# Kernel tuning notes

Measured on AMD Instinct MI355X. Metric: run time of the kernel, lower is better.

## Reference

```python
import jax, jax.numpy as jnp
import numpy as np

N_NODES = 50000
N_EDGES = 800000
D_IN = 128
D_HID = 128
BN_EPS = 1e-5


def _sage_mean(h, src, dst, w_self, w_neigh, b):
    # DGL SAGEConv('mean'): out = h @ W_self + mean_{neighbors}(h_src) @ W_neigh + bias
    msg = h[src]                                               # [E, D] gather
    ssum = jax.ops.segment_sum(msg, dst, num_segments=N_NODES)  # [N, D]
    deg = jax.ops.segment_sum(jnp.ones((src.shape[0],), h.dtype), dst,
                              num_segments=N_NODES)            # [N]
    mean = ssum / jnp.maximum(deg, 1.0)[:, None]
    return h @ w_self + mean @ w_neigh + b


def _bn_relu(h, gamma, beta):
    # BatchNorm1d with batch statistics (training-mode math), then ReLU.
    m = jnp.mean(h, axis=0)
    v = jnp.mean(jnp.square(h - m), axis=0)  # biased variance, as torch uses for normalization
    hn = (h - m) * jax.lax.rsqrt(v + BN_EPS) * gamma + beta
    return jax.nn.relu(hn)


def setup_inputs() -> dict:
    key = jax.random.key(0)
    ks = jax.random.split(key, 16)
    x = jax.random.normal(ks[0], (N_NODES, D_IN), dtype=jnp.float32)
    src = jax.random.randint(ks[1], (N_EDGES,), 0, N_NODES, dtype=jnp.int32)
    dst = jax.random.randint(ks[2], (N_EDGES,), 0, N_NODES, dtype=jnp.int32)
    s0 = 1.0 / np.sqrt(D_IN)
    s1 = 1.0 / np.sqrt(D_HID)
    inp = {
        'x': x, 'src': src, 'dst': dst,
        'W_self0': jax.random.uniform(ks[3], (D_IN, D_HID), jnp.float32, -s0, s0),
        'W_neigh0': jax.random.uniform(ks[4], (D_IN, D_HID), jnp.float32, -s0, s0),
        'b0': jnp.zeros((D_HID,), jnp.float32),
        'W_self1': jax.random.uniform(ks[5], (D_HID, D_HID), jnp.float32, -s1, s1),
        'W_neigh1': jax.random.uniform(ks[6], (D_HID, D_HID), jnp.float32, -s1, s1),
        'b1': jnp.zeros((D_HID,), jnp.float32),
        'W_self2': jax.random.uniform(ks[7], (D_HID, D_HID), jnp.float32, -s1, s1),
        'W_neigh2': jax.random.uniform(ks[8], (D_HID, D_HID), jnp.float32, -s1, s1),
        'b2': jnp.zeros((D_HID,), jnp.float32),
        'gamma0': jnp.ones((D_HID,), jnp.float32),
        'beta0': jnp.zeros((D_HID,), jnp.float32),
        'gamma1': jnp.ones((D_HID,), jnp.float32),
        'beta1': jnp.zeros((D_HID,), jnp.float32),
    }
    return inp


def reference(x, src, dst,
              W_self0, W_neigh0, b0,
              W_self1, W_neigh1, b1,
              W_self2, W_neigh2, b2,
              gamma0, beta0, gamma1, beta1):
    h = _sage_mean(x, src, dst, W_self0, W_neigh0, b0)
    h = _bn_relu(h, gamma0, beta0)  # dropout is identity in eval mode
    h = _sage_mean(h, src, dst, W_self1, W_neigh1, b1)
    h = _bn_relu(h, gamma1, beta1)
    h = _sage_mean(h, src, dst, W_self2, W_neigh2, b2)
    return h
```

## Files before the change

kernel.cpp:

```cpp
#include <hip/hip_runtime.h>

#define N_NODES 50000
#define N_EDGES 800000
#define D 128
#define BN_EPS 1e-5f

#define NBUCK 391
#define BSHIFT 7
#define S1_BLOCKS 256
#define EPB 3125
#define CVT_BLOCKS 6250
#define PACK_BLOCKS 384
#define NREP 16
#define NSLICE 8
#define SSHIFT 13
#define BN_BLOCKS 512

typedef __attribute__((ext_vector_type(8))) short bf16x8;
typedef __attribute__((ext_vector_type(4))) float f32x4;
typedef __attribute__((ext_vector_type(2))) float f32x2;

__device__ inline unsigned short f2bf(float f) {
    unsigned int u = __float_as_uint(f);
    u = (u + 0x7FFF + ((u >> 16) & 1)) >> 16;
    return (unsigned short)u;
}

__device__ inline float bf2f(unsigned short b) {
    return __uint_as_float(((unsigned)b) << 16);
}

__device__ __forceinline__ void acc_plain(f32x2* a, uint4 v) {
    unsigned w[4] = {v.x, v.y, v.z, v.w};
#pragma unroll
    for (int p = 0; p < 4; p++) {
        f32x2 f;
        f.x = __uint_as_float(w[p] << 16);
        f.y = __uint_as_float(w[p] & 0xffff0000u);
        a[p] += f;
    }
}


__global__ void fused_prep(const float* __restrict__ x, unsigned short* __restrict__ x16,
                           const int* __restrict__ dst, int* __restrict__ hist,
                           const float* __restrict__ Ws0, const float* __restrict__ Wn0,
                           const float* __restrict__ Ws1, const float* __restrict__ Wn1,
                           const float* __restrict__ Ws2, const float* __restrict__ Wn2,
                           unsigned short* __restrict__ Wf, float* __restrict__ statsg) {
    __shared__ int lh[NBUCK];
    const int bid = blockIdx.x, t = threadIdx.x;

    if (bid < CVT_BLOCKS) {
        int idx = bid * 256 + t;
        float4 v = ((const float4*)x)[idx];
        ushort4 o;
        o.x = f2bf(v.x); o.y = f2bf(v.y); o.z = f2bf(v.z); o.w = f2bf(v.w);
        ((ushort4*)x16)[idx] = o;
    } else if (bid < CVT_BLOCKS + S1_BLOCKS) {
        int blk = bid - CVT_BLOCKS;
        for (int i = t; i < NBUCK; i += 256) lh[i] = 0;
        __syncthreads();
        int e0 = blk * EPB;
        for (int i = 0; i < 13; i++) {
            int k = t + i * 256;
            if (k < EPB) atomicAdd(&lh[dst[e0 + k] >> BSHIFT], 1);
        }
        __syncthreads();
        for (int i = t; i < NBUCK; i += 256) hist[blk * NBUCK + i] = lh[i];
    } else {
        if (bid == CVT_BLOCKS + S1_BLOCKS) {
            for (int i = t; i < 2 * NREP * 256; i += 256) statsg[i] = 0.f;
        }
        int idx = (bid - (CVT_BLOCKS + S1_BLOCKS)) * 256 + t;
        if (idx < 3 * 32768) {
            int layer = idx >> 15;
            int rem = idx & 32767;
            int kt = rem >> 12;
            int nt = (rem >> 9) & 7;
            int lane = (rem >> 3) & 63;
            int j = rem & 7;
            int k = kt * 32 + (lane >> 4) * 8 + j;
            int n = nt * 16 + (lane & 15);
            const float* Wsrc;
            if (layer == 0) Wsrc = (k < 128) ? Ws0 : Wn0;
            else if (layer == 1) Wsrc = (k < 128) ? Ws1 : Wn1;
            else Wsrc = (k < 128) ? Ws2 : Wn2;
            Wf[idx] = f2bf(Wsrc[(k & 127) * D + n]);
        }
    }
}


__global__ void s2a(int* __restrict__ hist, int* __restrict__ bucketTotal) {
    __shared__ int s[S1_BLOCKS];
    int b = blockIdx.x, t = threadIdx.x;
    int v = hist[t * NBUCK + b];
    s[t] = v;
    __syncthreads();
    for (int off = 1; off < S1_BLOCKS; off <<= 1) {
        int x = (t >= off) ? s[t - off] : 0;
        __syncthreads();
        s[t] += x;
        __syncthreads();
    }
    hist[t * NBUCK + b] = s[t] - v;
    if (t == S1_BLOCKS - 1) bucketTotal[b] = s[t];
}


__global__ void s3_scatter(const int* __restrict__ src, const int* __restrict__ dst,
                           const int* __restrict__ hist, const int* __restrict__ bucketTotal,
                           int* __restrict__ bucketStart, unsigned int* __restrict__ rec) {
    __shared__ int sc[512];
    __shared__ int base[NBUCK];
    int blk = blockIdx.x, t = threadIdx.x;
    int i1 = t + 256;
    int v0 = (t < NBUCK) ? bucketTotal[t] : 0;
    int v1 = (i1 < NBUCK) ? bucketTotal[i1] : 0;
    sc[t] = v0; sc[i1] = v1;
    __syncthreads();
    for (int off = 1; off < 512; off <<= 1) {
        int x0 = (t >= off) ? sc[t - off] : 0;
        int x1 = (i1 >= off) ? sc[i1 - off] : 0;
        __syncthreads();
        sc[t] += x0; sc[i1] += x1;
        __syncthreads();
    }
    if (t < NBUCK)  base[t]  = (sc[t] - v0)  + hist[blk * NBUCK + t];
    if (i1 < NBUCK) base[i1] = (sc[i1] - v1) + hist[blk * NBUCK + i1];
    if (blk == 0) {
        if (t < NBUCK)  bucketStart[t]  = sc[t] - v0;
        if (i1 < NBUCK) bucketStart[i1] = sc[i1] - v1;
        if (t == 0) bucketStart[NBUCK] = N_EDGES;
    }
    __syncthreads();
    int e0 = blk * EPB;
    for (int i = 0; i < 13; i++) {
        int k = t + i * 256;
        if (k < EPB) {
            int e = e0 + k;
            int d = dst[e];
            int p = atomicAdd(&base[d >> BSHIFT], 1);
            rec[p] = ((unsigned)(d & 127) << 16) | (unsigned)src[e];
        }
    }
}


__global__ void s4_build(const unsigned int* __restrict__ rec, const int* __restrict__ bucketStart,
                         unsigned short* __restrict__ csr, int* __restrict__ degi,
                         int* __restrict__ offsets, float* __restrict__ inv_deg) {
    __shared__ int cnt[128 * NSLICE];
    __shared__ int exc[128 * NSLICE];
    __shared__ int lcur[128 * NSLICE];
    __shared__ int ls[256];
    int b = blockIdx.x, t = threadIdx.x;
    int start = bucketStart[b], end = bucketStart[b + 1];

    for (int i = t; i < 128 * NSLICE; i += 256) cnt[i] = 0;
    __syncthreads();
    for (int e = start + t; e < end; e += 256) {
        unsigned r = rec[e];
        int key = ((r >> 16) << 3) | ((r & 0xFFFFu) >> SSHIFT);
        atomicAdd(&cnt[key], 1);
    }
    __syncthreads();

    int c0 = cnt[4 * t], c1 = cnt[4 * t + 1], c2 = cnt[4 * t + 2], c3 = cnt[4 * t + 3];
    int sum4 = c0 + c1 + c2 + c3;
    ls[t] = sum4;
    __syncthreads();
    for (int off = 1; off < 256; off <<= 1) {
        int x = (t >= off) ? ls[t - off] : 0;
        __syncthreads();
        ls[t] += x;
        __syncthreads();
    }
    int base = ls[t] - sum4;
    exc[4 * t]     = base;
    exc[4 * t + 1] = base + c0;
    exc[4 * t + 2] = base + c0 + c1;
    exc[4 * t + 3] = base + c0 + c1 + c2;
    lcur[4 * t]     = start + base;
    lcur[4 * t + 1] = start + base + c0;
    lcur[4 * t + 2] = start + base + c0 + c1;
    lcur[4 * t + 3] = start + base + c0 + c1 + c2;
    __syncthreads();

    if (t < 128) {
        int node = (b << BSHIFT) + t;
        int e0 = exc[8 * t];
        int e1 = (t == 127) ? (end - start) : exc[8 * t + 8];
        int v = e1 - e0;
        if (node < N_NODES) {
            degi[node] = v;
            offsets[node] = start + e0;
            inv_deg[node] = 1.0f / (float)max(v, 1);
        }
    }
    __syncthreads();
    for (int e = start + t; e < end; e += 256) {
        unsigned r = rec[e];
        int key = ((r >> 16) << 3) | ((r & 0xFFFFu) >> SSHIFT);
        int p = atomicAdd(&lcur[key], 1);
        csr[p] = (unsigned short)(r & 0xFFFFu);
    }
}


__global__ void degsort(const int* __restrict__ degi, int* __restrict__ perm) {
    __shared__ int h[256];
    __shared__ int cur[256];
    int t = threadIdx.x;
    if (t < 256) h[t] = 0;
    __syncthreads();
    for (int i = t; i < N_NODES; i += 1024)
        atomicAdd(&h[255 - min(degi[i], 255)], 1);
    __syncthreads();
    int v = (t < 256) ? h[t] : 0;
    for (int off = 1; off < 256; off <<= 1) {
        int x = 0;
        if (t < 256 && t >= off) x = h[t - off];
        __syncthreads();
        if (t < 256) h[t] += x;
        __syncthreads();
    }
    if (t < 256) cur[t] = h[t] - v;
    __syncthreads();
    for (int i = t; i < N_NODES; i += 1024) {
        int b = 255 - min(degi[i], 255);
        perm[atomicAdd(&cur[b], 1)] = i;
    }
}


__global__ void bn_relu_apply(unsigned short* __restrict__ h,
                              const float* __restrict__ stats,
                              const float* __restrict__ gamma, const float* __restrict__ beta) {
    __shared__ float sc[128], sh[128];
    int t = threadIdx.x;
    if (t < 128) {
        const float invN = 1.0f / (float)N_NODES;
        float s = 0.f, q = 0.f;
#pragma unroll
        for (int r = 0; r < NREP; r++) {
            s += stats[r * 256 + t];
            q += stats[r * 256 + 128 + t];
        }
        float m = s * invN;
        float var = q * invN - m * m;
        float scv = rsqrtf(var + BN_EPS) * gamma[t];
        sc[t] = scv;
        sh[t] = beta[t] - m * scv;
    }
    __syncthreads();
    const int total = N_NODES * D / 8;
    for (int idx = blockIdx.x * 256 + t; idx < total; idx += BN_BLOCKS * 256) {
        uint4 v = ((const uint4*)h)[idx];
        int col0 = (idx & 15) * 8;
        unsigned w[4] = {v.x, v.y, v.z, v.w};
        unsigned ow[4];
#pragma unroll
        for (int p = 0; p < 4; p++) {
            float lo = __uint_as_float(w[p] << 16);
            float hi = __uint_as_float(w[p] & 0xffff0000u);
            float rlo = fmaxf(lo * sc[col0 + 2 * p]     + sh[col0 + 2 * p],     0.f);
            float rhi = fmaxf(hi * sc[col0 + 2 * p + 1] + sh[col0 + 2 * p + 1], 0.f);
            ow[p] = ((unsigned)f2bf(rhi) << 16) | f2bf(rlo);
        }
        uint4 o;
        o.x = ow[0]; o.y = ow[1]; o.z = ow[2]; o.w = ow[3];
        ((uint4*)h)[idx] = o;
    }
}


#define GATHER(k) (*(const uint4*)(hb + ((size_t)csr[beg + (k)] << 7)))

__global__ void aggregate16(const unsigned short* __restrict__ h16,
                            const unsigned short* __restrict__ csr, const int* __restrict__ offsets,
                            const int* __restrict__ degi, const float* __restrict__ inv_deg,
                            const int* __restrict__ perm,
                            unsigned short* __restrict__ mean16) {
    int t = threadIdx.x;
    int node = perm[blockIdx.x * 16 + (t >> 4)];
    int c = t & 15;
    const unsigned short* hb = h16 + c * 8;
    int beg = offsets[node], n = degi[node];
    f32x2 a[4];
#pragma unroll
    for (int j = 0; j < 4; j++) a[j] = (f32x2)(0.f);

    int i = 0;
    if (n >= 4) {
        uint4 v0 = GATHER(0), v1 = GATHER(1), v2 = GATHER(2), v3 = GATHER(3);
        for (i = 4; i + 3 < n; i += 4) {
            uint4 w0 = GATHER(i), w1 = GATHER(i + 1), w2 = GATHER(i + 2), w3 = GATHER(i + 3);
            acc_plain(a, v0); acc_plain(a, v1); acc_plain(a, v2); acc_plain(a, v3);
            v0 = w0; v1 = w1; v2 = w2; v3 = w3;
        }
        acc_plain(a, v0); acc_plain(a, v1); acc_plain(a, v2); acc_plain(a, v3);
    }
    for (; i < n; i++) { uint4 v = GATHER(i); acc_plain(a, v); }

    float w = inv_deg[node];
    uint4 o;
    o.x = ((unsigned)f2bf(a[0].y * w) << 16) | f2bf(a[0].x * w);
    o.y = ((unsigned)f2bf(a[1].y * w) << 16) | f2bf(a[1].x * w);
    o.z = ((unsigned)f2bf(a[2].y * w) << 16) | f2bf(a[2].x * w);
    o.w = ((unsigned)f2bf(a[3].y * w) << 16) | f2bf(a[3].x * w);
    *(uint4*)(mean16 + (size_t)node * D + c * 8) = o;
}


__global__ __launch_bounds__(256, 4) void sage_gemm(
    const unsigned short* __restrict__ h16, const unsigned short* __restrict__ mean16,
    const unsigned short* __restrict__ Wf, const float* __restrict__ bias,
    unsigned short* __restrict__ out16, float* __restrict__ outf,
    float* __restrict__ statsOut) {
    __shared__ unsigned short sWf[16384];
    __shared__ float sstat[256];
    const int t = threadIdx.x;
    const int lane = t & 63;
    const int m = lane & 15;
    const int quad = lane >> 4;
    const int wrow0 = blockIdx.x * 64 + (t >> 6) * 16;

    int arow = wrow0 + m;
    if (arow >= N_NODES) arow = N_NODES - 1;

    bf16x8 afr[8];
#pragma unroll
    for (int kt = 0; kt < 4; kt++)
        afr[kt] = *(const bf16x8*)(h16 + (size_t)arow * D + kt * 32 + quad * 8);
#pragma unroll
    for (int kt = 0; kt < 4; kt++)
        afr[4 + kt] = *(const bf16x8*)(mean16 + (size_t)arow * D + kt * 32 + quad * 8);

    const uint4* W4 = (const uint4*)Wf;
    uint4* S4 = (uint4*)sWf;
#pragma unroll
    for (int i = 0; i < 8; i++) S4[i * 256 + t] = W4[i * 256 + t];
    if (statsOut) sstat[t] = 0.f;
    __syncthreads();

    f32x4 acc[8];
#pragma unroll
    for (int i = 0; i < 8; i++) acc[i] = (f32x4)(0.f);

#pragma unroll
    for (int kt = 0; kt < 4; kt++) {
#pragma unroll
        for (int nt = 0; nt < 8; nt++) {
            bf16x8 bf = *(const bf16x8*)(sWf + ((kt * 8 + nt) * 64 + lane) * 8);
            acc[nt] = __builtin_amdgcn_mfma_f32_16x16x32_bf16(afr[kt], bf, acc[nt], 0, 0, 0);
        }
    }

    __syncthreads();
#pragma unroll
    for (int i = 0; i < 8; i++) S4[i * 256 + t] = W4[2048 + i * 256 + t];
    __syncthreads();

#pragma unroll
    for (int kt = 4; kt < 8; kt++) {
#pragma unroll
        for (int nt = 0; nt < 8; nt++) {
            bf16x8 bf = *(const bf16x8*)(sWf + (((kt - 4) * 8 + nt) * 64 + lane) * 8);
            acc[nt] = __builtin_amdgcn_mfma_f32_16x16x32_bf16(afr[kt], bf, acc[nt], 0, 0, 0);
        }
    }

    const bool do16 = (out16 != nullptr);
#pragma unroll
    for (int nt = 0; nt < 8; nt++) {
        int cidx = nt * 16 + m;
        float bv = bias[cidx];
        float s = 0.f, q = 0.f;
#pragma unroll
        for (int reg = 0; reg < 4; reg++) {
            int r = wrow0 + quad * 4 + reg;
            float v = acc[nt][reg] + bv;
            if (r < N_NODES) {
                if (do16) out16[(size_t)r * D + cidx] = f2bf(v);
                else      outf[(size_t)r * D + cidx] = v;
                s += v; q += v * v;
            }
        }
        if (statsOut) {
            s += __shfl_xor(s, 16); s += __shfl_xor(s, 32);
            q += __shfl_xor(q, 16); q += __shfl_xor(q, 32);
            if (quad == 0) {
                atomicAdd(&sstat[cidx], s);
                atomicAdd(&sstat[128 + cidx], q);
            }
        }
    }
    if (statsOut) {
        __syncthreads();
        atomicAdd(&statsOut[(blockIdx.x & (NREP - 1)) * 256 + t], sstat[t]);
    }
}


extern "C" void kernel_launch(void* const* d_in, const int* in_sizes, int n_in,
                              void* d_out, int out_size, void* d_ws, size_t ws_size,
                              hipStream_t stream) {
    const float* x   = (const float*)d_in[0];
    const int* src   = (const int*)d_in[1];
    const int* dst   = (const int*)d_in[2];
    const float* Ws0 = (const float*)d_in[3];
    const float* Wn0 = (const float*)d_in[4];
    const float* b0  = (const float*)d_in[5];
    const float* Ws1 = (const float*)d_in[6];
    const float* Wn1 = (const float*)d_in[7];
    const float* b1  = (const float*)d_in[8];
    const float* Ws2 = (const float*)d_in[9];
    const float* Wn2 = (const float*)d_in[10];
    const float* b2  = (const float*)d_in[11];
    const float* g0  = (const float*)d_in[12];
    const float* be0 = (const float*)d_in[13];
    const float* g1  = (const float*)d_in[14];
    const float* be1 = (const float*)d_in[15];

    char* base = (char*)d_ws;
    size_t NND = (size_t)N_NODES * D;
    unsigned short* X16    = (unsigned short*)base;
    unsigned short* H16    = (unsigned short*)(base + NND * 2);
    unsigned short* mean16 = (unsigned short*)(base + 2 * NND * 2);
    char* p = base + 6 * NND;
    unsigned short* Wf = (unsigned short*)p;  p += 3 * 32768 * 2;
    int* hist          = (int*)p;             p += (size_t)S1_BLOCKS * NBUCK * 4;
    int* bucketTotal   = (int*)p;             p += 1568;
    int* bucketStart   = (int*)p;             p += 1600;
    unsigned int* rec  = (unsigned int*)p;    p += (size_t)N_EDGES * 4;
    unsigned short* csr = (unsigned short*)p; p += (size_t)N_EDGES * 2;
    int* degi    = (int*)p;                   p += N_NODES * 4;
    int* offsets = (int*)p;                   p += N_NODES * 4;
    float* inv_deg = (float*)p;               p += N_NODES * 4;
    int* perm    = (int*)p;                   p += N_NODES * 4;
    float* stats   = (float*)p;               p += 2 * NREP * 256 * 4;
    float* stats0 = stats, *stats1 = stats + NREP * 256;

    fused_prep<<<CVT_BLOCKS + S1_BLOCKS + PACK_BLOCKS, 256, 0, stream>>>(
        x, X16, dst, hist, Ws0, Wn0, Ws1, Wn1, Ws2, Wn2, Wf, stats);
    s2a<<<NBUCK, 256, 0, stream>>>(hist, bucketTotal);
    s3_scatter<<<S1_BLOCKS, 256, 0, stream>>>(src, dst, hist, bucketTotal, bucketStart, rec);
    s4_build<<<NBUCK, 256, 0, stream>>>(rec, bucketStart, csr, degi, offsets, inv_deg);
    degsort<<<1, 1024, 0, stream>>>(degi, perm);

    const int AGG_B = (N_NODES + 15) / 16;
    const int GEMM_B = (N_NODES + 63) / 64;

    aggregate16<<<AGG_B, 256, 0, stream>>>(X16, csr, offsets, degi, inv_deg, perm, mean16);
    sage_gemm<<<GEMM_B, 256, 0, stream>>>(X16, mean16, Wf, b0, H16, nullptr, stats0);

    bn_relu_apply<<<BN_BLOCKS, 256, 0, stream>>>(H16, stats0, g0, be0);
    aggregate16<<<AGG_B, 256, 0, stream>>>(H16, csr, offsets, degi, inv_deg, perm, mean16);
    sage_gemm<<<GEMM_B, 256, 0, stream>>>(H16, mean16, Wf + 32768, b1, X16, nullptr, stats1);

    bn_relu_apply<<<BN_BLOCKS, 256, 0, stream>>>(X16, stats1, g1, be1);
    aggregate16<<<AGG_B, 256, 0, stream>>>(X16, csr, offsets, degi, inv_deg, perm, mean16);
    sage_gemm<<<GEMM_B, 256, 0, stream>>>(X16, mean16, Wf + 65536, b2, nullptr,
                                          (float*)d_out, nullptr);
}
```

Measured before the change: 312.9 us.

## Parallelize degree sort into multi-block histogram, scan and scatter kernels

Replaces the single-block degree counting sort with a three-kernel version: per-block histograms over 64 degree bins, one scan kernel that computes per-block, per-bin bases, and a multi-block scatter. The aim is to stop one 1024-thread block from walking all 50k nodes serially. In exchange it adds two extra kernel launches and coarsens the degree bins from 256 to 64, which changes the ordering for high-degree nodes. The order within a bin is still nondeterministic because of the shared-memory atomics.

```diff
diff --git a/kernel.cpp b/kernel.cpp
--- a/kernel.cpp
+++ b/kernel.cpp
@@ -15,6 +15,10 @@
 #define NSLICE 8
 #define SSHIFT 13
 #define BN_BLOCKS 512
+
+#define DS_BINS 64
+#define DS_BLOCKS 256
+#define DS_CHUNK 196
 
 typedef __attribute__((ext_vector_type(8))) short bf16x8;
 typedef __attribute__((ext_vector_type(4))) float f32x4;
@@ -209,28 +213,58 @@
 }
 
 
-__global__ void degsort(const int* __restrict__ degi, int* __restrict__ perm) {
-    __shared__ int h[256];
-    __shared__ int cur[256];
+__global__ void degsort_hist(const int* __restrict__ degi, int* __restrict__ hist2) {
+    __shared__ int h[DS_BINS];
+    int b = blockIdx.x, t = threadIdx.x;
+    if (t < DS_BINS) h[t] = 0;
+    __syncthreads();
+    int n0 = b * DS_CHUNK;
+    for (int i = t; i < DS_CHUNK; i += 256) {
+        int node = n0 + i;
+        if (node < N_NODES)
+            atomicAdd(&h[DS_BINS - 1 - min(degi[node], DS_BINS - 1)], 1);
+    }
+    __syncthreads();
+    if (t < DS_BINS) hist2[b * DS_BINS + t] = h[t];
+}
+
+__global__ void degsort_scan(const int* __restrict__ hist2, int* __restrict__ baseArr) {
+    __shared__ int tot[256];
     int t = threadIdx.x;
-    if (t < 256) h[t] = 0;
-    __syncthreads();
-    for (int i = t; i < N_NODES; i += 1024)
-        atomicAdd(&h[255 - min(degi[i], 255)], 1);
-    __syncthreads();
-    int v = (t < 256) ? h[t] : 0;
+    int s = 0;
+    for (int i = 0; i < 64; i++) {
+        int flat = t * 64 + i;
+        s += hist2[(flat & 255) * DS_BINS + (flat >> 8)];
+    }
+    tot[t] = s;
+    __syncthreads();
     for (int off = 1; off < 256; off <<= 1) {
-        int x = 0;
-        if (t < 256 && t >= off) x = h[t - off];
-        __syncthreads();
-        if (t < 256) h[t] += x;
-        __syncthreads();
-    }
-    if (t < 256) cur[t] = h[t] - v;
-    __syncthreads();
-    for (int i = t; i < N_NODES; i += 1024) {
-        int b = 255 - min(degi[i], 255);
-        perm[atomicAdd(&cur[b], 1)] = i;
+        int x = (t >= off) ? tot[t - off] : 0;
+        __syncthreads();
+        tot[t] += x;
+        __syncthreads();
+    }
+    int run = tot[t] - s;
+    for (int i = 0; i < 64; i++) {
+        int flat = t * 64 + i;
+        baseArr[flat] = run;
+        run += hist2[(flat & 255) * DS_BINS + (flat >> 8)];
+    }
+}
+
+__global__ void degsort_scatter(const int* __restrict__ degi, const int* __restrict__ baseArr,
+                                int* __restrict__ perm) {
+    __shared__ int lcur[DS_BINS];
+    int b = blockIdx.x, t = threadIdx.x;
+    if (t < DS_BINS) lcur[t] = baseArr[t * DS_BLOCKS + b];
+    __syncthreads();
+    int n0 = b * DS_CHUNK;
+    for (int i = t; i < DS_CHUNK; i += 256) {
+        int node = n0 + i;
+        if (node < N_NODES) {
+            int bin = DS_BINS - 1 - min(degi[node], DS_BINS - 1);
+            perm[atomicAdd(&lcur[bin], 1)] = node;
+        }
     }
 }
 
@@ -440,6 +474,8 @@
     int* offsets = (int*)p;                   p += N_NODES * 4;
     float* inv_deg = (float*)p;               p += N_NODES * 4;
     int* perm    = (int*)p;                   p += N_NODES * 4;
+    int* hist2   = (int*)p;                   p += DS_BLOCKS * DS_BINS * 4;
+    int* baseArr = (int*)p;                   p += DS_BLOCKS * DS_BINS * 4;
     float* stats   = (float*)p;               p += 2 * NREP * 256 * 4;
     float* stats0 = stats, *stats1 = stats + NREP * 256;
 
@@ -448,7 +484,9 @@
     s2a<<<NBUCK, 256, 0, stream>>>(hist, bucketTotal);
     s3_scatter<<<S1_BLOCKS, 256, 0, stream>>>(src, dst, hist, bucketTotal, bucketStart, rec);
     s4_build<<<NBUCK, 256, 0, stream>>>(rec, bucketStart, csr, degi, offsets, inv_deg);
-    degsort<<<1, 1024, 0, stream>>>(degi, perm);
+    degsort_hist<<<DS_BLOCKS, 256, 0, stream>>>(degi, hist2);
+    degsort_scan<<<1, 256, 0, stream>>>(hist2, baseArr);
+    degsort_scatter<<<DS_BLOCKS, 256, 0, stream>>>(degi, baseArr, perm);
 
     const int AGG_B = (N_NODES + 15) / 16;
     const int GEMM_B = (N_NODES + 63) / 64;
```

Result: faster. 287.5 us (-8.1%).
